# Performance work log

Hardware: AMD Instinct MI355X
Metric: run time of the kernel (lower is better)

## Reference

```python
import jax, jax.numpy as jnp
import numpy as np

B, S, H, NH = 2, 2048, 1024, 16
HD = H // NH  # head dim = 64


def setup_inputs() -> dict:
    key = jax.random.key(0)
    k_in, k_q, k_kv, k_o = jax.random.split(key, 4)
    scale = 0.02
    return {
        "inputs": jax.random.normal(k_in, (B, S, H), dtype=jnp.float32),
        "Wq": jax.random.normal(k_q, (H, H), dtype=jnp.float32) * scale,
        "bq": jnp.zeros((H,), dtype=jnp.float32),
        "Wkv": jax.random.normal(k_kv, (H, 2 * H), dtype=jnp.float32) * scale,
        "bkv": jnp.zeros((2 * H,), dtype=jnp.float32),
        "Wo": jax.random.normal(k_o, (H, H), dtype=jnp.float32) * scale,
        "bo": jnp.zeros((H,), dtype=jnp.float32),
    }


def reference(inputs, Wq, bq, Wkv, bkv, Wo, bo):
    b, s, h = inputs.shape
    q = inputs @ Wq + bq                      # [B,S,H]
    kv = inputs @ Wkv + bkv                   # [B,S,2H]
    k, v = kv[..., :h], kv[..., h:]           # each [B,S,H]
    q = q.reshape(b, s, NH, HD)
    k = k.reshape(b, s, NH, HD)
    v = v.reshape(b, s, NH, HD)
    inv_sqrt_d = jnp.asarray(1.0 / np.sqrt(HD), dtype=inputs.dtype)
    scores = jnp.einsum("bqhd,bkhd->bhqk", q, k) * inv_sqrt_d  # [B,NH,S,S]
    probs = jax.nn.softmax(scores, axis=-1)
    attended = jnp.einsum("bhqk,bkhd->bqhd", probs, v)         # [B,S,NH,HD]
    attended = attended.reshape(b, s, h)
    return attended @ Wo + bo
```

## Files before the change

### kernel.cpp

```cpp
#include <hip/hip_runtime.h>
#include <cstdint>

typedef __bf16 bf16;
typedef __attribute__((ext_vector_type(8))) __bf16 bf16x8;
typedef __attribute__((ext_vector_type(4))) __bf16 bf16v4;
typedef __attribute__((ext_vector_type(2))) __bf16 bf16x2;
typedef __attribute__((ext_vector_type(4))) float f32x4;
typedef __attribute__((ext_vector_type(16))) float f32x16;
typedef __attribute__((ext_vector_type(4))) unsigned u32x4;

#define MFMA16(a, b, c) __builtin_amdgcn_mfma_f32_16x16x32_bf16((a), (b), (c), 0, 0, 0)
#define MFMA32(a, b, c) __builtin_amdgcn_mfma_f32_32x32x16_bf16((a), (b), (c), 0, 0, 0)

#define BATCH 2
#define SLEN 2048
#define HDIM 1024
#define NHEAD 16
#define HEADD 64
#define MROWS (BATCH * SLEN)

#define CEXP 0.1803368801f

typedef __attribute__((address_space(3))) void lds_void;
typedef const __attribute__((address_space(1))) void glb_void;
__device__ __forceinline__ void load_lds16(const bf16* g, bf16* l) {
    __builtin_amdgcn_global_load_lds((glb_void*)g, (lds_void*)l, 16, 0, 0);
}

__device__ __forceinline__ void plswap(unsigned& a, unsigned& b) {
#if __has_builtin(__builtin_amdgcn_permlane32_swap)
    auto r = __builtin_amdgcn_permlane32_swap(a, b, false, false);
    a = r[0]; b = r[1];
#else
    asm volatile("v_permlane32_swap_b32 %0, %1" : "+v"(a), "+v"(b));
#endif
}

__device__ __forceinline__ unsigned cvtpk_bf16(float lo, float hi) {
    unsigned r;
    asm("v_cvt_pk_bf16_f32 %0, %1, %2" : "=v"(r) : "v"(lo), "v"(hi));
    return r;
}

__global__ __launch_bounds__(256) void prep_kernel(const float* __restrict__ X,
                                                   const float* __restrict__ Wq,
                                                   const float* __restrict__ Wkv,
                                                   const float* __restrict__ Wo,
                                                   const float* __restrict__ bq,
                                                   const float* __restrict__ bkv,
                                                   bf16* __restrict__ Xbf,
                                                   bf16* __restrict__ WqkvT,
                                                   bf16* __restrict__ WoT,
                                                   float* __restrict__ bqkv) {
    const int blk = blockIdx.x;
    const int tid = threadIdx.x;
    if (blk < 4096) {
        int i = (blk * 256 + tid) * 4;
        float4 v = *(const float4*)&X[i];
        bf16v4 o;
        o[0] = (bf16)v.x; o[1] = (bf16)v.y; o[2] = (bf16)v.z; o[3] = (bf16)v.w;
        *(bf16v4*)&Xbf[i] = o;
        return;
    }
    if (blk < 8192) {
        const float* in; bf16* out; int C, id;
        if (blk < 5120)      { in = Wq;  out = WqkvT;                C = 1024; id = blk - 4096; }
        else if (blk < 7168) { in = Wkv; out = WqkvT + 1024 * 1024;  C = 2048; id = blk - 5120; }
        else                 { in = Wo;  out = WoT;                  C = 1024; id = blk - 7168; }
        const int R = 1024;
        const int nbx = C / 32;
        const int j0 = (id % nbx) * 32, i0 = (id / nbx) * 32;
        const int tx = tid & 31, ty = tid >> 5;
        __shared__ float t[32][33];
        for (int r = ty; r < 32; r += 8)
            t[r][tx] = in[(size_t)(i0 + r) * C + j0 + tx];
        __syncthreads();
        for (int r = ty; r < 32; r += 8)
            out[(size_t)(j0 + r) * R + i0 + tx] = (bf16)t[tx][r];
        return;
    }
    int i = (blk - 8192) * 256 + tid;
    if (i < 3072) bqkv[i] = (i < 1024) ? bq[i] : bkv[i - 1024];
}

template <int BM, int BN, int EPI>
__global__ __launch_bounds__(256) void gemm2_kernel(const bf16* __restrict__ A,
                                                    const bf16* __restrict__ BT,
                                                    const float* __restrict__ bias,
                                                    bf16* __restrict__ oQ,
                                                    bf16* __restrict__ oK,
                                                    bf16* __restrict__ oVT,
                                                    float* __restrict__ oF, int K) {
    constexpr int WM = BM / 2, WN = BN / 2;
    constexpr int MT = WM / 16, NT = WN / 16;
    constexpr int NLD = BM / 64 + BN / 64;

    const int tid = threadIdx.x;
    const int lane = tid & 63, wid = tid >> 6;
    const int l15 = lane & 15, quad = lane >> 4;
    const int wm = (wid >> 1) * WM, wn = (wid & 1) * WN;
    const int m0 = blockIdx.y * BM, n0 = blockIdx.x * BN;

    __shared__ bf16 As[2][BM * 32];
    __shared__ bf16 Bs[2][BN * 32];

    f32x4 acc[MT][NT] = {};

    const bf16* Ag = A + (size_t)m0 * K;
    const bf16* Bg = BT + (size_t)n0 * K;
    const int arow = lane >> 2, acol = (lane & 3) * 8;

#define GSTAGE(buf, k0v) {                                                   \
        _Pragma("unroll")                                                    \
        for (int t = 0; t < BM / 64; ++t) {                                  \
            int tt = t * 4 + wid;                                            \
            load_lds16(Ag + (size_t)(tt * 16 + arow) * K + (k0v) + acol,     \
                       &As[buf][tt * 512]);                                  \
        }                                                                    \
        _Pragma("unroll")                                                    \
        for (int t = 0; t < BN / 64; ++t) {                                  \
            int tt = t * 4 + wid;                                            \
            load_lds16(Bg + (size_t)(tt * 16 + arow) * K + (k0v) + acol,     \
                       &Bs[buf][tt * 512]);                                  \
        }                                                                    \
    }

    GSTAGE(0, 0)

    const int NSTEP = K >> 5;
    for (int s = 0; s < NSTEP; ++s) {
        const int cur = s & 1;
        if (s < NSTEP - 1) {
            GSTAGE(cur ^ 1, (s + 1) * 32)
            if constexpr (NLD == 4)
                asm volatile("s_waitcnt vmcnt(4)" ::: "memory");
            else if constexpr (NLD == 3)
                asm volatile("s_waitcnt vmcnt(3)" ::: "memory");
            else
                asm volatile("s_waitcnt vmcnt(2)" ::: "memory");
        } else {
            asm volatile("s_waitcnt vmcnt(0)" ::: "memory");
        }
        __builtin_amdgcn_s_barrier();

        bf16x8 af[MT], bfr[NT];
#pragma unroll
        for (int i = 0; i < MT; ++i)
            af[i] = *(const bf16x8*)&As[cur][(wm + i * 16 + l15) * 32 + quad * 8];
#pragma unroll
        for (int j = 0; j < NT; ++j)
            bfr[j] = *(const bf16x8*)&Bs[cur][(wn + j * 16 + l15) * 32 + quad * 8];
#pragma unroll
        for (int i = 0; i < MT; ++i)
#pragma unroll
            for (int j = 0; j < NT; ++j)
                acc[i][j] = MFMA16(af[i], bfr[j], acc[i][j]);

        asm volatile("s_waitcnt lgkmcnt(0)" ::: "memory");
        __builtin_amdgcn_s_barrier();
    }
#undef GSTAGE

#pragma unroll
    for (int i = 0; i < MT; ++i) {
#pragma unroll
        for (int j = 0; j < NT; ++j) {
            const int mb = m0 + wm + i * 16 + quad * 4;
            const int n = n0 + wn + j * 16 + l15;
            const float bv = bias[n];
            if (EPI == 2) {
                float* o = oF + (size_t)mb * 1024 + n;
#pragma unroll
                for (int r = 0; r < 4; ++r) o[(size_t)r * 1024] = acc[i][j][r] + bv;
            } else if (n0 < 1024) {
#pragma unroll
                for (int r = 0; r < 4; ++r)
                    oQ[(size_t)(mb + r) * 1024 + n] = (bf16)((acc[i][j][r] + bv) * CEXP);
            } else if (n0 < 2048) {
#pragma unroll
                for (int r = 0; r < 4; ++r)
                    oK[(size_t)(mb + r) * 1024 + (n - 1024)] = (bf16)(acc[i][j][r] + bv);
            } else {
                const int hd = n - 2048;
                const int bb = mb >> 11, ss = mb & 2047;
                bf16v4 pk;
#pragma unroll
                for (int r = 0; r < 4; ++r) pk[r] = (bf16)(acc[i][j][r] + bv);
                *(bf16v4*)&oVT[((size_t)(bb << 10) + hd) * 2048 + ss] = pk;
            }
        }
    }
}

__device__ __forceinline__ void sm_half(f32x16 sa, f32x16 sb, float& l_lane,
                                        bf16x8* pf) {
    unsigned wA[2][4], wB[2][4];
#pragma unroll
    for (int m = 0; m < 2; ++m) {
        const f32x16 s = m ? sb : sa;
#pragma unroll
        for (int g = 0; g < 4; ++g) {
            float p0 = __builtin_amdgcn_exp2f(s[g * 4 + 0]);
            float p1 = __builtin_amdgcn_exp2f(s[g * 4 + 1]);
            float p2 = __builtin_amdgcn_exp2f(s[g * 4 + 2]);
            float p3 = __builtin_amdgcn_exp2f(s[g * 4 + 3]);
            l_lane += (p0 + p1) + (p2 + p3);
            wA[m][g] = cvtpk_bf16(p0, p1);
            wB[m][g] = cvtpk_bf16(p2, p3);
        }
    }
#pragma unroll
    for (int s = 0; s < 4; ++s) {
        const int m = s >> 1, qa = (s & 1) * 2, qb = qa + 1;
        unsigned x0 = wA[m][qa], x2 = wA[m][qb];
        unsigned x1 = wB[m][qa], x3 = wB[m][qb];
        plswap(x0, x2);
        plswap(x1, x3);
        u32x4 fw;
        fw[0] = x0; fw[1] = x1; fw[2] = x2; fw[3] = x3;
        pf[s] = __builtin_bit_cast(bf16x8, fw);
    }
}

__global__ __launch_bounds__(256) void attn8_kernel(const bf16* __restrict__ Q,
                                                    const bf16* __restrict__ K,
                                                    const bf16* __restrict__ VT,
                                                    bf16* __restrict__ O) {
    const int bid = blockIdx.x;
    const int xcd = bid & 7, j = bid >> 3;
    const int bh = xcd * 4 + (j >> 4);
    const int q0 = (j & 15) * 128;
    const int b = bh >> 4, head = bh & 15;
    const int tid = threadIdx.x;
    const int lane = tid & 63, wid = tid >> 6;
    const int l31 = lane & 31, hh = lane >> 5;

    __shared__ bf16 Ks[2][128 * 64];
    __shared__ bf16 VTs[2][64 * 128];

    const int qw = q0 + wid * 32;
    bf16x8 qf[4];
#pragma unroll
    for (int kd = 0; kd < 4; ++kd)
        qf[kd] = *(const bf16x8*)&Q[(size_t)(b * SLEN + qw + l31) * HDIM +
                                    head * 64 + kd * 16 + hh * 8];

    f32x16 o_acc[2] = {};
    const f32x16 ZC = {};
    float l_lane = 0.f;

    const bf16* Kg = K + (size_t)b * SLEN * HDIM + head * 64;
    const bf16* Vg = VT + (size_t)bh * 64 * SLEN;

    const int r8 = lane >> 3, p8 = lane & 7;
    const int r16 = lane >> 4, p16 = lane & 15;

    const int ph = (j & 1) << 3;

#define STAGE(buf, ktv) {                                                          \
        const int k0_ = (((ktv) + ph) & 15) * 128;                                 \
        _Pragma("unroll")                                                          \
        for (int pass = 0; pass < 4; ++pass) {                                     \
            const int rbk = pass * 32 + wid * 8;                                   \
            load_lds16(Kg + (size_t)(k0_ + rbk + r8) * HDIM +                      \
                           ((p8 ^ ((rbk + r8) & 7)) * 8),                          \
                       &Ks[buf][rbk * 64]);                                        \
            const int rbv = pass * 16 + wid * 4;                                   \
            load_lds16(Vg + (size_t)(rbv + r16) * SLEN + k0_ +                     \
                           ((p16 ^ ((rbv + r16) & 15)) * 8),                       \
                       &VTs[buf][rbv * 128]);                                      \
        } }

    STAGE(0, 0)

    for (int kt = 0; kt < 16; ++kt) {
        const int cur = kt & 1;
        if (kt < 15) {
            STAGE(cur ^ 1, kt + 1)
            asm volatile("s_waitcnt vmcnt(8)" ::: "memory");
        } else {
            asm volatile("s_waitcnt vmcnt(0)" ::: "memory");
        }
        __builtin_amdgcn_s_barrier();

        const bf16* Kc = &Ks[cur][0];
        const bf16* Vc = &VTs[cur][0];

        f32x16 s00, s01, s10, s11;
        __builtin_amdgcn_s_setprio(1);
#define QK_STEP(sv, h, m, kd, Cin) {                                       \
        const int key_ = ((h) * 2 + (m)) * 32 + l31;                       \
        const int c_ = ((kd) * 2 + hh) ^ (key_ & 7);                       \
        bf16x8 kf_ = *(const bf16x8*)&Kc[key_ * 64 + c_ * 8];              \
        sv = MFMA32(kf_, qf[kd], Cin); }
        QK_STEP(s00, 0, 0, 0, ZC)
        QK_STEP(s01, 0, 1, 0, ZC)
        QK_STEP(s10, 1, 0, 0, ZC)
        QK_STEP(s11, 1, 1, 0, ZC)
#pragma unroll
        for (int kd = 1; kd < 4; ++kd) {
            QK_STEP(s00, 0, 0, kd, s00)
            QK_STEP(s01, 0, 1, kd, s01)
            QK_STEP(s10, 1, 0, kd, s10)
            QK_STEP(s11, 1, 1, kd, s11)
        }
        __builtin_amdgcn_s_setprio(0);

        bf16x8 pf0[4], pf1[4];
        sm_half(s00, s01, l_lane, pf0);

        __builtin_amdgcn_s_setprio(1);
#pragma unroll
        for (int s = 0; s < 4; ++s)
#pragma unroll
            for (int dt = 0; dt < 2; ++dt) {
                const int d = dt * 32 + l31;
                const int cc = (s * 2 + hh) ^ (d & 15);
                bf16x8 vf = *(const bf16x8*)&Vc[d * 128 + cc * 8];
                o_acc[dt] = MFMA32(vf, pf0[s], o_acc[dt]);
            }
        __builtin_amdgcn_s_setprio(0);

        sm_half(s10, s11, l_lane, pf1);

        __builtin_amdgcn_s_setprio(1);
#pragma unroll
        for (int s = 0; s < 4; ++s)
#pragma unroll
            for (int dt = 0; dt < 2; ++dt) {
                const int d = dt * 32 + l31;
                const int cc = ((4 + s) * 2 + hh) ^ (d & 15);
                bf16x8 vf = *(const bf16x8*)&Vc[d * 128 + cc * 8];
                o_acc[dt] = MFMA32(vf, pf1[s], o_acc[dt]);
            }
        __builtin_amdgcn_s_setprio(0);

        asm volatile("" ::: "memory");
        __builtin_amdgcn_s_barrier();
    }

    const float l_full = l_lane + __shfl_xor(l_lane, 32, 64);
    const float inv = 1.f / l_full;
    bf16* orow = O + (size_t)(b * SLEN + qw + l31) * HDIM + head * 64;
#pragma unroll
    for (int mt = 0; mt < 2; ++mt)
#pragma unroll
        for (int g = 0; g < 4; ++g) {
            bf16v4 pk;
#pragma unroll
            for (int r = 0; r < 4; ++r) pk[r] = (bf16)(o_acc[mt][g * 4 + r] * inv);
            *(bf16v4*)&orow[mt * 32 + g * 8 + 4 * hh] = pk;
        }
}

extern "C" void kernel_launch(void* const* d_in, const int* in_sizes, int n_in,
                              void* d_out, int out_size, void* d_ws, size_t ws_size,
                              hipStream_t stream) {
    const float* X   = (const float*)d_in[0];
    const float* Wq  = (const float*)d_in[1];
    const float* bq  = (const float*)d_in[2];
    const float* Wkv = (const float*)d_in[3];
    const float* bkv = (const float*)d_in[4];
    const float* Wo  = (const float*)d_in[5];
    const float* bo  = (const float*)d_in[6];
    float* out = (float*)d_out;

    char* ws = (char*)d_ws;
    bf16* Xbf   = (bf16*)(ws);
    bf16* WqkvT = (bf16*)(ws + (8ull << 20));
    bf16* WoT   = (bf16*)(ws + (14ull << 20));
    float* bqkv = (float*)(ws + (16ull << 20));
    bf16* Qbf   = (bf16*)(ws + (17ull << 20));
    bf16* Kbf   = (bf16*)(ws + (25ull << 20));
    bf16* VTbf  = (bf16*)(ws + (33ull << 20));
    bf16* Abf   = (bf16*)(ws + (41ull << 20));

    prep_kernel<<<8204, 256, 0, stream>>>(X, Wq, Wkv, Wo, bq, bkv, Xbf, WqkvT, WoT, bqkv);

    gemm2_kernel<128, 128, 1><<<dim3(3072 / 128, MROWS / 128), 256, 0, stream>>>(
        Xbf, WqkvT, bqkv, Qbf, Kbf, VTbf, nullptr, 1024);

    attn8_kernel<<<512, 256, 0, stream>>>(Qbf, Kbf, VTbf, Abf);

    gemm2_kernel<128, 64, 2><<<dim3(1024 / 64, MROWS / 128), 256, 0, stream>>>(
        Abf, WoT, bo, nullptr, nullptr, nullptr, out, 1024);
}
```

Measured before the change: 192.3 us.

## Split attention over key halves with a combine pass, remap GEMM tiles across XCDs

The attention kernel now splits the key dimension into two halves, doubling the grid to 1024 blocks, and shrinks the K/V tiles to 64 keys. It writes unnormalized fp32 partial outputs and row sums, which a new combine kernel adds and normalizes into bf16. This is valid because the softmax here uses a fixed exponent offset (CEXP) with no running max, so partials add directly. Separately, GEMM block indices are remapped so consecutive tiles land on the same XCD, to improve L2 locality. The split adds an extra launch and fp32 partial traffic of about 32 MB of writes and reads.

```diff
diff --git a/kernel.cpp b/kernel.cpp
--- a/kernel.cpp
+++ b/kernel.cpp
@@ -99,7 +99,11 @@
     const int lane = tid & 63, wid = tid >> 6;
     const int l15 = lane & 15, quad = lane >> 4;
     const int wm = (wid >> 1) * WM, wn = (wid & 1) * WN;
-    const int m0 = blockIdx.y * BM, n0 = blockIdx.x * BN;
+
+    const int lid = blockIdx.y * gridDim.x + blockIdx.x;
+    const int per = (gridDim.x * gridDim.y) >> 3;
+    const int wg = (lid & 7) * per + (lid >> 3);
+    const int m0 = (wg / gridDim.x) * BM, n0 = (wg % gridDim.x) * BN;
 
     __shared__ bf16 As[2][BM * 32];
     __shared__ bf16 Bs[2][BN * 32];
@@ -222,21 +226,24 @@
     }
 }
 
-__global__ __launch_bounds__(256) void attn8_kernel(const bf16* __restrict__ Q,
-                                                    const bf16* __restrict__ K,
-                                                    const bf16* __restrict__ VT,
-                                                    bf16* __restrict__ O) {
+__global__ __launch_bounds__(256) void attn10_kernel(const bf16* __restrict__ Q,
+                                                     const bf16* __restrict__ K,
+                                                     const bf16* __restrict__ VT,
+                                                     float* __restrict__ Opart,
+                                                     float* __restrict__ Lpart) {
     const int bid = blockIdx.x;
     const int xcd = bid & 7, j = bid >> 3;
-    const int bh = xcd * 4 + (j >> 4);
-    const int q0 = (j & 15) * 128;
+    const int bh = xcd * 4 + (j >> 5);
+    const int rest = j & 31;
+    const int split = rest >> 4;
+    const int q0 = (rest & 15) * 128;
     const int b = bh >> 4, head = bh & 15;
     const int tid = threadIdx.x;
     const int lane = tid & 63, wid = tid >> 6;
     const int l31 = lane & 31, hh = lane >> 5;
 
-    __shared__ bf16 Ks[2][128 * 64];
-    __shared__ bf16 VTs[2][64 * 128];
+    __shared__ bf16 Ks[2][64 * 64];
+    __shared__ bf16 VTs[2][64 * 64];
 
     const int qw = q0 + wid * 32;
     bf16x8 qf[4];
@@ -253,22 +260,22 @@
     const bf16* Vg = VT + (size_t)bh * 64 * SLEN;
 
     const int r8 = lane >> 3, p8 = lane & 7;
-    const int r16 = lane >> 4, p16 = lane & 15;
-
-    const int ph = (j & 1) << 3;
+
+    const int ph = (j & 3) << 2;
+    const int kbase = split * 1024;
 
 #define STAGE(buf, ktv) {                                                          \
-        const int k0_ = (((ktv) + ph) & 15) * 128;                                 \
+        const int k0_ = kbase + (((ktv) + ph) & 15) * 64;                          \
         _Pragma("unroll")                                                          \
-        for (int pass = 0; pass < 4; ++pass) {                                     \
+        for (int pass = 0; pass < 2; ++pass) {                                     \
             const int rbk = pass * 32 + wid * 8;                                   \
             load_lds16(Kg + (size_t)(k0_ + rbk + r8) * HDIM +                      \
                            ((p8 ^ ((rbk + r8) & 7)) * 8),                          \
                        &Ks[buf][rbk * 64]);                                        \
-            const int rbv = pass * 16 + wid * 4;                                   \
-            load_lds16(Vg + (size_t)(rbv + r16) * SLEN + k0_ +                     \
-                           ((p16 ^ ((rbv + r16) & 15)) * 8),                       \
-                       &VTs[buf][rbv * 128]);                                      \
+            const int rbv = pass * 32 + wid * 8;                                   \
+            load_lds16(Vg + (size_t)(rbv + r8) * SLEN + k0_ +                      \
+                           ((p8 ^ ((rbv + r8) & 7)) * 8),                          \
+                       &VTs[buf][rbv * 64]);                                       \
         } }
 
     STAGE(0, 0)
@@ -277,7 +284,7 @@
         const int cur = kt & 1;
         if (kt < 15) {
             STAGE(cur ^ 1, kt + 1)
-            asm volatile("s_waitcnt vmcnt(8)" ::: "memory");
+            asm volatile("s_waitcnt vmcnt(4)" ::: "memory");
         } else {
             asm volatile("s_waitcnt vmcnt(0)" ::: "memory");
         }
@@ -286,28 +293,24 @@
         const bf16* Kc = &Ks[cur][0];
         const bf16* Vc = &VTs[cur][0];
 
-        f32x16 s00, s01, s10, s11;
+        f32x16 s0, s1;
         __builtin_amdgcn_s_setprio(1);
-#define QK_STEP(sv, h, m, kd, Cin) {                                       \
-        const int key_ = ((h) * 2 + (m)) * 32 + l31;                       \
+#define QK_STEP(sv, m, kd, Cin) {                                          \
+        const int key_ = (m) * 32 + l31;                                   \
         const int c_ = ((kd) * 2 + hh) ^ (key_ & 7);                       \
         bf16x8 kf_ = *(const bf16x8*)&Kc[key_ * 64 + c_ * 8];              \
         sv = MFMA32(kf_, qf[kd], Cin); }
-        QK_STEP(s00, 0, 0, 0, ZC)
-        QK_STEP(s01, 0, 1, 0, ZC)
-        QK_STEP(s10, 1, 0, 0, ZC)
-        QK_STEP(s11, 1, 1, 0, ZC)
+        QK_STEP(s0, 0, 0, ZC)
+        QK_STEP(s1, 1, 0, ZC)
 #pragma unroll
         for (int kd = 1; kd < 4; ++kd) {
-            QK_STEP(s00, 0, 0, kd, s00)
-            QK_STEP(s01, 0, 1, kd, s01)
-            QK_STEP(s10, 1, 0, kd, s10)
-            QK_STEP(s11, 1, 1, kd, s11)
+            QK_STEP(s0, 0, kd, s0)
+            QK_STEP(s1, 1, kd, s1)
         }
         __builtin_amdgcn_s_setprio(0);
 
-        bf16x8 pf0[4], pf1[4];
-        sm_half(s00, s01, l_lane, pf0);
+        bf16x8 pf[4];
+        sm_half(s0, s1, l_lane, pf);
 
         __builtin_amdgcn_s_setprio(1);
 #pragma unroll
@@ -315,42 +318,51 @@
 #pragma unroll
             for (int dt = 0; dt < 2; ++dt) {
                 const int d = dt * 32 + l31;
-                const int cc = (s * 2 + hh) ^ (d & 15);
-                bf16x8 vf = *(const bf16x8*)&Vc[d * 128 + cc * 8];
-                o_acc[dt] = MFMA32(vf, pf0[s], o_acc[dt]);
+                const int cc = (s * 2 + hh) ^ (d & 7);
+                bf16x8 vf = *(const bf16x8*)&Vc[d * 64 + cc * 8];
+                o_acc[dt] = MFMA32(vf, pf[s], o_acc[dt]);
             }
         __builtin_amdgcn_s_setprio(0);
 
-        sm_half(s10, s11, l_lane, pf1);
-
-        __builtin_amdgcn_s_setprio(1);
-#pragma unroll
-        for (int s = 0; s < 4; ++s)
-#pragma unroll
-            for (int dt = 0; dt < 2; ++dt) {
-                const int d = dt * 32 + l31;
-                const int cc = ((4 + s) * 2 + hh) ^ (d & 15);
-                bf16x8 vf = *(const bf16x8*)&Vc[d * 128 + cc * 8];
-                o_acc[dt] = MFMA32(vf, pf1[s], o_acc[dt]);
-            }
-        __builtin_amdgcn_s_setprio(0);
-
-        asm volatile("" ::: "memory");
+        asm volatile("s_waitcnt lgkmcnt(0)" ::: "memory");
+        __builtin_amdgcn_sched_barrier(0);
         __builtin_amdgcn_s_barrier();
     }
 
-    const float l_full = l_lane + __shfl_xor(l_lane, 32, 64);
-    const float inv = 1.f / l_full;
-    bf16* orow = O + (size_t)(b * SLEN + qw + l31) * HDIM + head * 64;
+    const float l_half = l_lane + __shfl_xor(l_lane, 32, 64);
+
+    const int qrow = (bh << 11) + qw + l31;
+    float* op = Opart + ((size_t)split << 22) + (size_t)qrow * 64;
 #pragma unroll
     for (int mt = 0; mt < 2; ++mt)
 #pragma unroll
-        for (int g = 0; g < 4; ++g) {
-            bf16v4 pk;
-#pragma unroll
-            for (int r = 0; r < 4; ++r) pk[r] = (bf16)(o_acc[mt][g * 4 + r] * inv);
-            *(bf16v4*)&orow[mt * 32 + g * 8 + 4 * hh] = pk;
-        }
+        for (int gq = 0; gq < 4; ++gq) {
+            float4 v4;
+            v4.x = o_acc[mt][gq * 4 + 0];
+            v4.y = o_acc[mt][gq * 4 + 1];
+            v4.z = o_acc[mt][gq * 4 + 2];
+            v4.w = o_acc[mt][gq * 4 + 3];
+            *(float4*)&op[mt * 32 + gq * 8 + 4 * hh] = v4;
+        }
+    if (hh == 0) Lpart[(split << 16) + qrow] = l_half;
+}
+
+__global__ __launch_bounds__(256) void combine_kernel(const float* __restrict__ Opart,
+                                                      const float* __restrict__ Lpart,
+                                                      bf16* __restrict__ A) {
+    const int idx = blockIdx.x * 256 + threadIdx.x;
+    const int qrow = idx >> 4, dq = (idx & 15) << 2;
+    const float l = Lpart[qrow] + Lpart[(1 << 16) + qrow];
+    const float4 a = *(const float4*)&Opart[(size_t)idx * 4];
+    const float4 c = *(const float4*)&Opart[(1ull << 22) + (size_t)idx * 4];
+    const float inv = 1.f / l;
+    bf16v4 o;
+    o[0] = (bf16)((a.x + c.x) * inv);
+    o[1] = (bf16)((a.y + c.y) * inv);
+    o[2] = (bf16)((a.z + c.z) * inv);
+    o[3] = (bf16)((a.w + c.w) * inv);
+    const int bh = qrow >> 11, q = qrow & 2047;
+    *(bf16v4*)&A[((size_t)((bh >> 4) * SLEN + q)) * HDIM + (bh & 15) * 64 + dq] = o;
 }
 
 extern "C" void kernel_launch(void* const* d_in, const int* in_sizes, int n_in,
@@ -374,13 +386,16 @@
     bf16* Kbf   = (bf16*)(ws + (25ull << 20));
     bf16* VTbf  = (bf16*)(ws + (33ull << 20));
     bf16* Abf   = (bf16*)(ws + (41ull << 20));
+    float* Opart = (float*)(ws + (49ull << 20));
+    float* Lpart = (float*)(ws + (81ull << 20));
 
     prep_kernel<<<8204, 256, 0, stream>>>(X, Wq, Wkv, Wo, bq, bkv, Xbf, WqkvT, WoT, bqkv);
 
     gemm2_kernel<128, 128, 1><<<dim3(3072 / 128, MROWS / 128), 256, 0, stream>>>(
         Xbf, WqkvT, bqkv, Qbf, Kbf, VTbf, nullptr, 1024);
 
-    attn8_kernel<<<512, 256, 0, stream>>>(Qbf, Kbf, VTbf, Abf);
+    attn10_kernel<<<1024, 256, 0, stream>>>(Qbf, Kbf, VTbf, Opart, Lpart);
+    combine_kernel<<<4096, 256, 0, stream>>>(Opart, Lpart, Abf);
 
     gemm2_kernel<128, 64, 2><<<dim3(1024 / 64, MROWS / 128), 256, 0, stream>>>(
         Abf, WoT, bo, nullptr, nullptr, nullptr, out, 1024);
```

After: 202.8 us. 1.05x slower.
